# Optimization experiments

Measured on AMD Instinct MI355X. Metric: run time of the kernel, lower is better.

Reference implementation:

```python
import jax, jax.numpy as jnp
import numpy as np

N, D, R, E = 50000, 128, 16, 1600000


def rgcn_conv(x, W, root, bias, src, dst, rel):
    """PyG-style RGCNConv (aggr='mean', root weight + bias).
    out[i] = x[i] @ root + bias + sum_r mean_{j in N_r(i)} x[j] @ W_r
    Aggregate-then-transform: segment-mean per (relation, dst) then contract with W.
    """
    n, d = x.shape
    seg = rel * n + dst  # combined (relation, dst-node) segment id
    msg_sum = jax.ops.segment_sum(x[src], seg, num_segments=R * n).reshape(R, n, d)
    cnt = jax.ops.segment_sum(jnp.ones_like(src, dtype=x.dtype), seg, num_segments=R * n).reshape(R, n, 1)
    msg = msg_sum / jnp.maximum(cnt, 1.0)  # mean aggregation (0 when no edges)
    return jnp.einsum('rnd,rde->ne', msg, W) + x @ root + bias


def setup_inputs() -> dict:
    key = jax.random.key(0)
    ks = jax.random.split(key, 9)
    x = jax.random.normal(ks[0], (N, D), dtype=jnp.float32)
    edge_index = jax.random.randint(ks[1], (2, E), 0, N, dtype=jnp.int64)
    edge_type = jax.random.randint(ks[2], (E,), 0, R, dtype=jnp.int64)
    s = 1.0 / np.sqrt(D)
    W1 = jax.random.normal(ks[3], (R, D, D), dtype=jnp.float32) * s
    root1 = jax.random.normal(ks[4], (D, D), dtype=jnp.float32) * s
    b1 = jnp.zeros((D,), dtype=jnp.float32)
    W2 = jax.random.normal(ks[5], (R, D, D), dtype=jnp.float32) * s
    root2 = jax.random.normal(ks[6], (D, D), dtype=jnp.float32) * s
    b2 = jnp.zeros((D,), dtype=jnp.float32)
    return {"x": x, "edge_index": edge_index, "edge_type": edge_type,
            "W1": W1, "root1": root1, "b1": b1,
            "W2": W2, "root2": root2, "b2": b2}


def reference(x, edge_index, edge_type, W1, root1, b1, W2, root2, b2):
    src, dst = edge_index[0], edge_index[1]
    # layer 1: RGCN -> ReLU -> Dropout (identity in eval mode)
    h = jax.nn.relu(rgcn_conv(x, W1, root1, b1, src, dst, edge_type))
    # layer 2: RGCN -> ReLU
    h = jax.nn.relu(rgcn_conv(h, W2, root2, b2, src, dst, edge_type))
    return h
```

## Files before the change

kernel.cpp:

```cpp
#include <hip/hip_runtime.h>


#define ND 128
#define NR 16
#define KPB 4096

typedef __attribute__((ext_vector_type(8))) short bf16x8;
typedef __attribute__((ext_vector_type(4))) float f32x4;

__device__ __forceinline__ unsigned short f2b(float f) {
    unsigned u = __float_as_uint(f);
    u += 0x7FFFu + ((u >> 16) & 1u);
    return (unsigned short)(u >> 16);
}

__global__ __launch_bounds__(256) void coarse_hist(
    const int* __restrict__ dst, const int* __restrict__ rel,
    int* __restrict__ coarse_cnt, int E, int N, int NBK)
{
    __shared__ int h[1024];
    const int t = threadIdx.x;
    for (int i = t; i < NBK; i += 256) h[i] = 0;
    __syncthreads();
#pragma unroll
    for (int q = 0; q < 16; ++q) {
        int e = blockIdx.x * KPB + q * 256 + t;
        if (e < E) {
            int key = rel[e] * N + dst[e];
            atomicAdd(&h[key >> 12], 1);
        }
    }
    __syncthreads();
    for (int i = t; i < NBK; i += 256)
        if (h[i]) atomicAdd(&coarse_cnt[i], h[i]);
}

__global__ __launch_bounds__(1024) void coarse_scan(
    const int* __restrict__ coarse_cnt, int* __restrict__ cscan,
    int* __restrict__ coarse_cursor, int NBK, int E)
{
    __shared__ int sdata[1024];
    const int t = threadIdx.x;
    int v = (t < NBK) ? coarse_cnt[t] : 0;
    sdata[t] = v;
    __syncthreads();
    for (int off = 1; off < 1024; off <<= 1) {
        int tmp = (t >= off) ? sdata[t - off] : 0;
        __syncthreads();
        sdata[t] += tmp;
        __syncthreads();
    }
    if (t < NBK) {
        int excl = sdata[t] - v;
        cscan[t] = excl;
        coarse_cursor[t] = excl;
    }
    if (t == 0) cscan[NBK] = E;
}

__global__ __launch_bounds__(256) void fillA(
    const int* __restrict__ src, const int* __restrict__ dst,
    const int* __restrict__ rel, int* __restrict__ coarse_cursor,
    uint2* __restrict__ coarse_buf, int E, int N, int NBK)
{
    __shared__ uint2 pairs[KPB];
    __shared__ int h[1024];
    const int t = threadIdx.x;
    for (int i = t; i < NBK; i += 256) h[i] = 0;
    __syncthreads();
#pragma unroll
    for (int q = 0; q < 16; ++q) {
        int e = blockIdx.x * KPB + q * 256 + t;
        unsigned key = 0xFFFFFFFFu, sv = 0;
        if (e < E) {
            key = (unsigned)(rel[e] * N + dst[e]);
            sv = (unsigned)src[e];
            atomicAdd(&h[key >> 12], 1);
        }
        pairs[q * 256 + t] = make_uint2(sv, key);
    }
    __syncthreads();
    for (int i = t; i < NBK; i += 256) {
        int c = h[i];
        h[i] = c ? atomicAdd(&coarse_cursor[i], c) : 0;
    }
    __syncthreads();
#pragma unroll
    for (int q = 0; q < 16; ++q) {
        uint2 p = pairs[q * 256 + t];
        if (p.y != 0xFFFFFFFFu) {
            int pos = atomicAdd(&h[p.y >> 12], 1);
            coarse_buf[pos] = p;
        }
    }
}

__global__ __launch_bounds__(256) void fillB(
    const uint2* __restrict__ coarse_buf, const int* __restrict__ cscan,
    int* __restrict__ seg_off, float* __restrict__ cnt_inv,
    int* __restrict__ sorted_src, int M, int E, int NBK)
{
    __shared__ int cnt[KPB];
    __shared__ int w[256];
    const int t = threadIdx.x;
    const int b = blockIdx.x;
    const int kbase = b << 12;
    const int nkeys = min(KPB, M - kbase);
    const int r0 = cscan[b], r1 = cscan[b + 1];

    for (int i = t; i < KPB; i += 256) cnt[i] = 0;
    __syncthreads();
    for (int e = r0 + t; e < r1; e += 256)
        atomicAdd(&cnt[coarse_buf[e].y - kbase], 1);
    __syncthreads();
    for (int i = t; i < nkeys; i += 256)
        cnt_inv[kbase + i] = 1.0f / fmaxf((float)cnt[i], 1.0f);
    int s = 0;
#pragma unroll
    for (int j = 0; j < 16; ++j) s += cnt[t * 16 + j];
    w[t] = s;
    __syncthreads();
    for (int off = 1; off < 256; off <<= 1) {
        int tmp = (t >= off) ? w[t - off] : 0;
        __syncthreads();
        w[t] += tmp;
        __syncthreads();
    }
    int run = r0 + w[t] - s;
#pragma unroll
    for (int j = 0; j < 16; ++j) {
        int i = t * 16 + j;
        int c = cnt[i];
        cnt[i] = run;
        if (i < nkeys) seg_off[kbase + i] = run;
        run += c;
    }
    if (b == NBK - 1 && t == 0) seg_off[M] = E;
    __syncthreads();
    for (int e = r0 + t; e < r1; e += 256) {
        uint2 p = coarse_buf[e];
        int pos = atomicAdd(&cnt[p.y - kbase], 1);
        sorted_src[pos] = (int)p.x;
    }
}

__global__ __launch_bounds__(256) void conv_x_kernel(
    const float* __restrict__ x, unsigned short* __restrict__ xb, int n4)
{
    int i = blockIdx.x * 256 + threadIdx.x;
    if (i >= n4) return;
    float4 v = ((const float4*)x)[i];
    uint2 o;
    o.x = (unsigned)f2b(v.x) | ((unsigned)f2b(v.y) << 16);
    o.y = (unsigned)f2b(v.z) | ((unsigned)f2b(v.w) << 16);
    ((uint2*)xb)[i] = o;
}

__global__ __launch_bounds__(256) void conv_w_kernel(
    const float* __restrict__ W, const float* __restrict__ root,
    unsigned short* __restrict__ Wt)
{
    int t = blockIdx.x * 256 + threadIdx.x;
    if (t >= 17 * 2048) return;
    int mat = t >> 11;
    int f = t & 2047;
    int lane = f & 63;
    int ctkt = f >> 6;
    int kt = ctkt >> 3;
    int ct = ctkt & 7;
    int n = ct * 16 + (lane & 15);
    int k = kt * 32 + (lane >> 4) * 8;
    const float* s = (mat < 16) ? (W + (size_t)mat * 16384) : root;
    uint4 o;
    o.x = (unsigned)f2b(s[(size_t)(k + 0) * ND + n]) | ((unsigned)f2b(s[(size_t)(k + 1) * ND + n]) << 16);
    o.y = (unsigned)f2b(s[(size_t)(k + 2) * ND + n]) | ((unsigned)f2b(s[(size_t)(k + 3) * ND + n]) << 16);
    o.z = (unsigned)f2b(s[(size_t)(k + 4) * ND + n]) | ((unsigned)f2b(s[(size_t)(k + 5) * ND + n]) << 16);
    o.w = (unsigned)f2b(s[(size_t)(k + 6) * ND + n]) | ((unsigned)f2b(s[(size_t)(k + 7) * ND + n]) << 16);
    *(uint4*)(Wt + (size_t)t * 8) = o;
}

__global__ __launch_bounds__(256) void gather_mean(
    const unsigned short* __restrict__ A,
    const int* __restrict__ seg_off,
    const int* __restrict__ sorted_src,
    const float* __restrict__ cnt_inv,
    unsigned short* __restrict__ msg,
    int N, int r0, int ccN)
{
    int g = blockIdx.x * 16 + (threadIdx.x >> 4);
    if (g >= ccN) return;
    int l = threadIdx.x & 15;
    int s = r0 * N + g;
    int b0 = seg_off[s], e1 = seg_off[s + 1];
    float a0 = 0.f, a1 = 0.f, a2 = 0.f, a3 = 0.f, a4 = 0.f, a5 = 0.f, a6 = 0.f, a7 = 0.f;
    int e = b0;
    for (; e + 2 <= e1; e += 2) {
        int s0 = sorted_src[e];
        int s1 = sorted_src[e + 1];
        uint4 u0 = *(const uint4*)(A + (size_t)s0 * ND + l * 8);
        uint4 u1 = *(const uint4*)(A + (size_t)s1 * ND + l * 8);
        a0 += __uint_as_float(u0.x << 16); a1 += __uint_as_float(u0.x & 0xFFFF0000u);
        a2 += __uint_as_float(u0.y << 16); a3 += __uint_as_float(u0.y & 0xFFFF0000u);
        a4 += __uint_as_float(u0.z << 16); a5 += __uint_as_float(u0.z & 0xFFFF0000u);
        a6 += __uint_as_float(u0.w << 16); a7 += __uint_as_float(u0.w & 0xFFFF0000u);
        a0 += __uint_as_float(u1.x << 16); a1 += __uint_as_float(u1.x & 0xFFFF0000u);
        a2 += __uint_as_float(u1.y << 16); a3 += __uint_as_float(u1.y & 0xFFFF0000u);
        a4 += __uint_as_float(u1.z << 16); a5 += __uint_as_float(u1.z & 0xFFFF0000u);
        a6 += __uint_as_float(u1.w << 16); a7 += __uint_as_float(u1.w & 0xFFFF0000u);
    }
    if (e < e1) {
        int s0 = sorted_src[e];
        uint4 u0 = *(const uint4*)(A + (size_t)s0 * ND + l * 8);
        a0 += __uint_as_float(u0.x << 16); a1 += __uint_as_float(u0.x & 0xFFFF0000u);
        a2 += __uint_as_float(u0.y << 16); a3 += __uint_as_float(u0.y & 0xFFFF0000u);
        a4 += __uint_as_float(u0.z << 16); a5 += __uint_as_float(u0.z & 0xFFFF0000u);
        a6 += __uint_as_float(u0.w << 16); a7 += __uint_as_float(u0.w & 0xFFFF0000u);
    }
    float inv = cnt_inv[s];
    uint4 o;
    o.x = (unsigned)f2b(a0 * inv) | ((unsigned)f2b(a1 * inv) << 16);
    o.y = (unsigned)f2b(a2 * inv) | ((unsigned)f2b(a3 * inv) << 16);
    o.z = (unsigned)f2b(a4 * inv) | ((unsigned)f2b(a5 * inv) << 16);
    o.w = (unsigned)f2b(a6 * inv) | ((unsigned)f2b(a7 * inv) << 16);
    *(uint4*)(msg + (size_t)g * ND + l * 8) = o;
}

__global__ __launch_bounds__(256) void gemm_mfma(
    const unsigned short* __restrict__ msg,
    const unsigned short* __restrict__ xb,
    const unsigned short* __restrict__ Wt,
    const float* __restrict__ bias,
    float* __restrict__ acc_buf,
    unsigned short* __restrict__ out_bf,
    float* __restrict__ out_f32,
    int N, int c0, int cc, int include_root, int load_acc, int finalize)
{
    __shared__ __align__(16) unsigned short Bs[2048 * 8];
    const int tid = threadIdx.x;
    const int lane = tid & 63;
    const int wv = tid >> 6;
    const int quad = lane >> 4;
    const int l16 = lane & 15;
    const int m0 = blockIdx.x * 64 + wv * 16;
    const int arow = m0 + l16;

    f32x4 acc[8];
    if (load_acc) {
#pragma unroll
        for (int ct = 0; ct < 8; ++ct)
#pragma unroll
            for (int rg = 0; rg < 4; ++rg) {
                int r = m0 + quad * 4 + rg;
                acc[ct][rg] = (r < N) ? acc_buf[(size_t)r * ND + ct * 16 + l16] : 0.f;
            }
    } else {
#pragma unroll
        for (int ct = 0; ct < 8; ++ct) { f32x4 z = {0.f, 0.f, 0.f, 0.f}; acc[ct] = z; }
    }

    for (int rel = include_root ? -1 : 0; rel < cc; ++rel) {
        const unsigned short* A = (rel < 0) ? xb : msg + (size_t)rel * N * ND;
        const int mat = (rel < 0) ? 16 : (c0 + rel);
        const uint4* Bsrc = (const uint4*)(Wt + (size_t)mat * 2048 * 8);

        bf16x8 a[4];
#pragma unroll
        for (int kt = 0; kt < 4; ++kt) {
            bf16x8 z = {0, 0, 0, 0, 0, 0, 0, 0};
            a[kt] = (arow < N) ? *(const bf16x8*)(A + (size_t)arow * ND + kt * 32 + quad * 8) : z;
        }

        __syncthreads();
#pragma unroll
        for (int i = 0; i < 8; ++i)
            ((uint4*)Bs)[tid + i * 256] = Bsrc[tid + i * 256];
        __syncthreads();

#pragma unroll
        for (int kt = 0; kt < 4; ++kt) {
#pragma unroll
            for (int ct = 0; ct < 8; ++ct) {
                bf16x8 b = *(const bf16x8*)(Bs + (size_t)((kt * 8 + ct) * 64 + lane) * 8);
                acc[ct] = __builtin_amdgcn_mfma_f32_16x16x32_bf16(a[kt], b, acc[ct], 0, 0, 0);
            }
        }
    }

    if (!finalize) {
#pragma unroll
        for (int ct = 0; ct < 8; ++ct)
#pragma unroll
            for (int rg = 0; rg < 4; ++rg) {
                int r = m0 + quad * 4 + rg;
                if (r < N) acc_buf[(size_t)r * ND + ct * 16 + l16] = acc[ct][rg];
            }
    } else {
#pragma unroll
        for (int ct = 0; ct < 8; ++ct) {
            float bb = bias[ct * 16 + l16];
#pragma unroll
            for (int rg = 0; rg < 4; ++rg) {
                int r = m0 + quad * 4 + rg;
                if (r < N) {
                    float v = fmaxf(acc[ct][rg] + bb, 0.f);
                    if (out_bf) out_bf[(size_t)r * ND + ct * 16 + l16] = f2b(v);
                    else        out_f32[(size_t)r * ND + ct * 16 + l16] = v;
                }
            }
        }
    }
}

extern "C" void kernel_launch(void* const* d_in, const int* in_sizes, int n_in,
                              void* d_out, int out_size, void* d_ws, size_t ws_size,
                              hipStream_t stream) {
    const float* x     = (const float*)d_in[0];
    const int*   eidx  = (const int*)d_in[1];
    const int*   etype = (const int*)d_in[2];
    const float* W1    = (const float*)d_in[3];
    const float* root1 = (const float*)d_in[4];
    const float* b1    = (const float*)d_in[5];
    const float* W2    = (const float*)d_in[6];
    const float* root2 = (const float*)d_in[7];
    const float* b2    = (const float*)d_in[8];
    float* out = (float*)d_out;

    const int N = in_sizes[0] / ND;
    const int E = in_sizes[2];
    const int M = NR * N;
    const int NBK = (M + KPB - 1) / KPB;

    const int* src = eidx;
    const int* dst = eidx + E;

    char* p = (char*)d_ws;
    auto carve = [&](size_t bytes) { char* q = p; p += (bytes + 255) & ~(size_t)255; return q; };
    unsigned short* h_bf    = (unsigned short*)carve((size_t)N * ND * 2);
    unsigned short* x_bf    = (unsigned short*)carve((size_t)N * ND * 2);
    unsigned short* Wt1     = (unsigned short*)carve((size_t)17 * 2048 * 8 * 2);
    unsigned short* Wt2     = (unsigned short*)carve((size_t)17 * 2048 * 8 * 2);
    int*   seg_off          = (int*)  carve((size_t)(M + 1) * 4);
    float* cnt_inv          = (float*)carve((size_t)M * 4);
    int*   sorted_src       = (int*)  carve((size_t)E * 4);
    int*   coarse_cnt       = (int*)  carve(1024 * 4);
    int*   cscan            = (int*)  carve(1025 * 4);
    int*   coarse_cursor    = (int*)  carve(1024 * 4);

    size_t fixed = (size_t)(p - (char*)d_ws);
    size_t remain = (ws_size > fixed) ? ws_size - fixed : 0;
    size_t chunk_bytes = (size_t)N * ND * 2;
    size_t acc_bytes   = (size_t)N * ND * 4;
    int C = 2;
    if (remain >= 16 * chunk_bytes + 512) C = 16;
    else if (remain >= 8 * chunk_bytes + acc_bytes + 512) C = 8;
    else if (remain >= 4 * chunk_bytes + acc_bytes + 512) C = 4;
    uint2* coarse_buf       = (uint2*)p;
    unsigned short* msg     = (unsigned short*)carve((size_t)C * chunk_bytes);
    float* acc              = (float*)((C < 16) ? carve(acc_bytes) : (char*)p);

    const int eb4 = (E + KPB - 1) / KPB;
    const int gemm_blocks = (N + 63) / 64;

    hipMemsetAsync(coarse_cnt, 0, 1024 * 4, stream);
    coarse_hist<<<eb4, 256, 0, stream>>>(dst, etype, coarse_cnt, E, N, NBK);
    coarse_scan<<<1, 1024, 0, stream>>>(coarse_cnt, cscan, coarse_cursor, NBK, E);
    fillA<<<eb4, 256, 0, stream>>>(src, dst, etype, coarse_cursor, coarse_buf, E, N, NBK);
    fillB<<<NBK, 256, 0, stream>>>(coarse_buf, cscan, seg_off, cnt_inv, sorted_src, M, E, NBK);

    conv_x_kernel<<<((N * ND / 4) + 255) / 256, 256, 0, stream>>>(x, x_bf, N * ND / 4);
    conv_w_kernel<<<(17 * 2048 + 255) / 256, 256, 0, stream>>>(W1, root1, Wt1);
    conv_w_kernel<<<(17 * 2048 + 255) / 256, 256, 0, stream>>>(W2, root2, Wt2);

    for (int layer = 0; layer < 2; ++layer) {
        const unsigned short* A  = (layer == 0) ? x_bf : h_bf;
        const unsigned short* Wt = (layer == 0) ? Wt1  : Wt2;
        const float* biasp       = (layer == 0) ? b1   : b2;

        for (int c0 = 0; c0 < NR; c0 += C) {
            int cc = (NR - c0 < C) ? (NR - c0) : C;
            int ccN = cc * N;
            gather_mean<<<(ccN + 15) / 16, 256, 0, stream>>>(
                A, seg_off, sorted_src, cnt_inv, msg, N, c0, ccN);
            int fin = (c0 + cc == NR) ? 1 : 0;
            gemm_mfma<<<gemm_blocks, 256, 0, stream>>>(
                msg, A, Wt, biasp, acc,
                (fin && layer == 0) ? h_bf : (unsigned short*)nullptr,
                (fin && layer == 1) ? out : (float*)nullptr,
                N, c0, cc, c0 == 0 ? 1 : 0, c0 > 0 ? 1 : 0, fin);
        }
    }
}
```

Before: 521.1 us.

## Split GEMM output columns across wave pairs and load weights directly into LDS

Each block of the MFMA GEMM now covers 32 rows instead of 64. Pairs of waves share a 16-row tile, each wave computing half of the output columns, which halves the accumulator registers per wave and doubles the block count. The launch bound now requests more resident blocks per CU. Weight tiles are copied with global_load_lds straight into shared memory instead of passing through registers, and final fp32 outputs use nontemporal stores. The trade-off is that each block now loads the full 32KB weight tile to produce half as many rows, doubling total weight traffic through LDS. The A fragments are also loaded redundantly by both waves of a pair.

```diff
diff --git a/kernel.cpp b/kernel.cpp
--- a/kernel.cpp
+++ b/kernel.cpp
@@ -12,6 +12,12 @@
     unsigned u = __float_as_uint(f);
     u += 0x7FFFu + ((u >> 16) & 1u);
     return (unsigned short)(u >> 16);
+}
+
+__device__ __forceinline__ void gload16(const unsigned short* g, unsigned short* l) {
+    __builtin_amdgcn_global_load_lds(
+        (__attribute__((address_space(1))) void*)g,
+        (__attribute__((address_space(3))) void*)l, 16, 0, 0);
 }
 
 __global__ __launch_bounds__(256) void coarse_hist(
@@ -225,7 +231,7 @@
     *(uint4*)(msg + (size_t)g * ND + l * 8) = o;
 }
 
-__global__ __launch_bounds__(256) void gemm_mfma(
+__global__ __launch_bounds__(256, 5) void gemm_mfma(
     const unsigned short* __restrict__ msg,
     const unsigned short* __restrict__ xb,
     const unsigned short* __restrict__ Wt,
@@ -239,72 +245,83 @@
     const int tid = threadIdx.x;
     const int lane = tid & 63;
     const int wv = tid >> 6;
+    const int rg = wv >> 1;
+    const int ch = wv & 1;
     const int quad = lane >> 4;
     const int l16 = lane & 15;
-    const int m0 = blockIdx.x * 64 + wv * 16;
+    const int m0 = blockIdx.x * 32 + rg * 16;
     const int arow = m0 + l16;
 
-    f32x4 acc[8];
+    f32x4 acc[4];
     if (load_acc) {
 #pragma unroll
-        for (int ct = 0; ct < 8; ++ct)
-#pragma unroll
-            for (int rg = 0; rg < 4; ++rg) {
-                int r = m0 + quad * 4 + rg;
-                acc[ct][rg] = (r < N) ? acc_buf[(size_t)r * ND + ct * 16 + l16] : 0.f;
+        for (int c = 0; c < 4; ++c) {
+            int ct = ch * 4 + c;
+#pragma unroll
+            for (int rgi = 0; rgi < 4; ++rgi) {
+                int r = m0 + quad * 4 + rgi;
+                acc[c][rgi] = (r < N) ? acc_buf[(size_t)r * ND + ct * 16 + l16] : 0.f;
             }
+        }
     } else {
 #pragma unroll
-        for (int ct = 0; ct < 8; ++ct) { f32x4 z = {0.f, 0.f, 0.f, 0.f}; acc[ct] = z; }
-    }
-
-    for (int rel = include_root ? -1 : 0; rel < cc; ++rel) {
-        const unsigned short* A = (rel < 0) ? xb : msg + (size_t)rel * N * ND;
+        for (int c = 0; c < 4; ++c) { f32x4 z = {0.f, 0.f, 0.f, 0.f}; acc[c] = z; }
+    }
+
+    const int rel0 = include_root ? -1 : 0;
+    const bf16x8 zfrag = {0, 0, 0, 0, 0, 0, 0, 0};
+
+    for (int rel = rel0; rel < cc; ++rel) {
+        const unsigned short* A = (rel < 0) ? xb : msg + (size_t)rel * (size_t)N * ND;
         const int mat = (rel < 0) ? 16 : (c0 + rel);
-        const uint4* Bsrc = (const uint4*)(Wt + (size_t)mat * 2048 * 8);
+        const unsigned short* Bsrc = Wt + (size_t)mat * 2048 * 8;
 
         bf16x8 a[4];
 #pragma unroll
         for (int kt = 0; kt < 4; ++kt) {
-            bf16x8 z = {0, 0, 0, 0, 0, 0, 0, 0};
-            a[kt] = (arow < N) ? *(const bf16x8*)(A + (size_t)arow * ND + kt * 32 + quad * 8) : z;
+            const bf16x8* ap = (const bf16x8*)(A + (size_t)arow * ND + kt * 32 + quad * 8);
+            a[kt] = (arow < N) ? *ap : zfrag;
         }
 
         __syncthreads();
 #pragma unroll
         for (int i = 0; i < 8; ++i)
-            ((uint4*)Bs)[tid + i * 256] = Bsrc[tid + i * 256];
+            gload16(Bsrc + (size_t)(tid + i * 256) * 8, &Bs[(size_t)(tid + i * 256) * 8]);
         __syncthreads();
 
 #pragma unroll
         for (int kt = 0; kt < 4; ++kt) {
 #pragma unroll
-            for (int ct = 0; ct < 8; ++ct) {
+            for (int c = 0; c < 4; ++c) {
+                int ct = ch * 4 + c;
                 bf16x8 b = *(const bf16x8*)(Bs + (size_t)((kt * 8 + ct) * 64 + lane) * 8);
-                acc[ct] = __builtin_amdgcn_mfma_f32_16x16x32_bf16(a[kt], b, acc[ct], 0, 0, 0);
+                acc[c] = __builtin_amdgcn_mfma_f32_16x16x32_bf16(a[kt], b, acc[c], 0, 0, 0);
             }
         }
     }
 
     if (!finalize) {
 #pragma unroll
-        for (int ct = 0; ct < 8; ++ct)
-#pragma unroll
-            for (int rg = 0; rg < 4; ++rg) {
-                int r = m0 + quad * 4 + rg;
-                if (r < N) acc_buf[(size_t)r * ND + ct * 16 + l16] = acc[ct][rg];
+        for (int c = 0; c < 4; ++c) {
+            int ct = ch * 4 + c;
+#pragma unroll
+            for (int rgi = 0; rgi < 4; ++rgi) {
+                int r = m0 + quad * 4 + rgi;
+                if (r < N) acc_buf[(size_t)r * ND + ct * 16 + l16] = acc[c][rgi];
             }
+        }
     } else {
 #pragma unroll
-        for (int ct = 0; ct < 8; ++ct) {
+        for (int c = 0; c < 4; ++c) {
+            int ct = ch * 4 + c;
             float bb = bias[ct * 16 + l16];
 #pragma unroll
-            for (int rg = 0; rg < 4; ++rg) {
-                int r = m0 + quad * 4 + rg;
+            for (int rgi = 0; rgi < 4; ++rgi) {
+                int r = m0 + quad * 4 + rgi;
                 if (r < N) {
-                    float v = fmaxf(acc[ct][rg] + bb, 0.f);
+                    float v = fmaxf(acc[c][rgi] + bb, 0.f);
                     if (out_bf) out_bf[(size_t)r * ND + ct * 16 + l16] = f2b(v);
-                    else        out_f32[(size_t)r * ND + ct * 16 + l16] = v;
+                    else        __builtin_nontemporal_store(v, &out_f32[(size_t)r * ND + ct * 16 + l16]);
                 }
             }
         }
@@ -359,7 +376,7 @@
     float* acc              = (float*)((C < 16) ? carve(acc_bytes) : (char*)p);
 
     const int eb4 = (E + KPB - 1) / KPB;
-    const int gemm_blocks = (N + 63) / 64;
+    const int gemm_blocks = (N + 31) / 32;
 
     hipMemsetAsync(coarse_cnt, 0, 1024 * 4, stream);
     coarse_hist<<<eb4, 256, 0, stream>>>(dst, etype, coarse_cnt, E, N, NBK);
```

Measured after the change: 547.5 us. 5.1% more time.

## Double-buffer weight tiles in LDS with async global-to-LDS loads in GEMM

Applied to the files above, without the earlier changes.

Rewrites the per-relation loop of the MFMA GEMM as a two-stage software pipeline. Two LDS buffers are used, and the next relation's weight tile is loaded with global_load_lds (plus the next A fragments into registers) while the current one is being multiplied. This hides global-load latency behind MFMA work. It doubles the LDS footprint per block, which can lower occupancy, and it relies on the barrier waiting for the async LDS loads. The final fp32 output store is also switched to nontemporal.

```diff
diff --git a/kernel.cpp b/kernel.cpp
--- a/kernel.cpp
+++ b/kernel.cpp
@@ -12,6 +12,12 @@
     unsigned u = __float_as_uint(f);
     u += 0x7FFFu + ((u >> 16) & 1u);
     return (unsigned short)(u >> 16);
+}
+
+__device__ __forceinline__ void gload16(const unsigned short* g, unsigned short* l) {
+    __builtin_amdgcn_global_load_lds(
+        (__attribute__((address_space(1))) void*)g,
+        (__attribute__((address_space(3))) void*)l, 16, 0, 0);
 }
 
 __global__ __launch_bounds__(256) void coarse_hist(
@@ -225,6 +231,32 @@
     *(uint4*)(msg + (size_t)g * ND + l * 8) = o;
 }
 
+#define PREFETCH(ph, BS, areg) do {                                              \
+    const int rel_ = rel0 + (ph);                                                \
+    const unsigned short* A_ = (rel_ < 0) ? xb : msg + (size_t)rel_ * (size_t)N * ND; \
+    const int mat_ = (rel_ < 0) ? 16 : (c0 + rel_);                              \
+    const unsigned short* Bsrc_ = Wt + (size_t)mat_ * 2048 * 8;                  \
+    _Pragma("unroll")                                                            \
+    for (int i_ = 0; i_ < 8; ++i_)                                               \
+        gload16(Bsrc_ + (size_t)(tid + i_ * 256) * 8, BS + (size_t)(tid + i_ * 256) * 8); \
+    _Pragma("unroll")                                                            \
+    for (int kt_ = 0; kt_ < 4; ++kt_) {                                          \
+        const bf16x8* ap_ = (const bf16x8*)(A_ + (size_t)arow * ND + kt_ * 32 + quad * 8); \
+        areg[kt_] = (arow < N) ? *ap_ : zfrag;                                   \
+    }                                                                            \
+} while (0)
+
+#define COMPUTE(BS, areg) do {                                                   \
+    _Pragma("unroll")                                                            \
+    for (int kt_ = 0; kt_ < 4; ++kt_) {                                          \
+        _Pragma("unroll")                                                        \
+        for (int ct_ = 0; ct_ < 8; ++ct_) {                                      \
+            bf16x8 b_ = *(const bf16x8*)(BS + (size_t)((kt_ * 8 + ct_) * 64 + lane) * 8); \
+            acc[ct_] = __builtin_amdgcn_mfma_f32_16x16x32_bf16(areg[kt_], b_, acc[ct_], 0, 0, 0); \
+        }                                                                        \
+    }                                                                            \
+} while (0)
+
 __global__ __launch_bounds__(256) void gemm_mfma(
     const unsigned short* __restrict__ msg,
     const unsigned short* __restrict__ xb,
@@ -235,7 +267,8 @@
     float* __restrict__ out_f32,
     int N, int c0, int cc, int include_root, int load_acc, int finalize)
 {
-    __shared__ __align__(16) unsigned short Bs[2048 * 8];
+    __shared__ __align__(16) unsigned short Bs0[2048 * 8];
+    __shared__ __align__(16) unsigned short Bs1[2048 * 8];
     const int tid = threadIdx.x;
     const int lane = tid & 63;
     const int wv = tid >> 6;
@@ -258,32 +291,26 @@
         for (int ct = 0; ct < 8; ++ct) { f32x4 z = {0.f, 0.f, 0.f, 0.f}; acc[ct] = z; }
     }
 
-    for (int rel = include_root ? -1 : 0; rel < cc; ++rel) {
-        const unsigned short* A = (rel < 0) ? xb : msg + (size_t)rel * N * ND;
-        const int mat = (rel < 0) ? 16 : (c0 + rel);
-        const uint4* Bsrc = (const uint4*)(Wt + (size_t)mat * 2048 * 8);
-
-        bf16x8 a[4];
-#pragma unroll
-        for (int kt = 0; kt < 4; ++kt) {
-            bf16x8 z = {0, 0, 0, 0, 0, 0, 0, 0};
-            a[kt] = (arow < N) ? *(const bf16x8*)(A + (size_t)arow * ND + kt * 32 + quad * 8) : z;
-        }
-
-        __syncthreads();
-#pragma unroll
-        for (int i = 0; i < 8; ++i)
-            ((uint4*)Bs)[tid + i * 256] = Bsrc[tid + i * 256];
-        __syncthreads();
-
-#pragma unroll
-        for (int kt = 0; kt < 4; ++kt) {
-#pragma unroll
-            for (int ct = 0; ct < 8; ++ct) {
-                bf16x8 b = *(const bf16x8*)(Bs + (size_t)((kt * 8 + ct) * 64 + lane) * 8);
-                acc[ct] = __builtin_amdgcn_mfma_f32_16x16x32_bf16(a[kt], b, acc[ct], 0, 0, 0);
-            }
-        }
+    const int rel0 = include_root ? -1 : 0;
+    const int P = cc - rel0;
+    const bf16x8 zfrag = {0, 0, 0, 0, 0, 0, 0, 0};
+    bf16x8 a0[4], a1[4];
+
+    PREFETCH(0, Bs0, a0);
+    int p = 0;
+    for (; p + 2 <= P; p += 2) {
+        __syncthreads();
+        if (p + 1 < P) { PREFETCH(p + 1, Bs1, a1); }
+        __builtin_amdgcn_sched_barrier(0);
+        COMPUTE(Bs0, a0);
+        __syncthreads();
+        if (p + 2 < P) { PREFETCH(p + 2, Bs0, a0); }
+        __builtin_amdgcn_sched_barrier(0);
+        COMPUTE(Bs1, a1);
+    }
+    if (p < P) {
+        __syncthreads();
+        COMPUTE(Bs0, a0);
     }
 
     if (!finalize) {
@@ -304,7 +331,7 @@
                 if (r < N) {
                     float v = fmaxf(acc[ct][rg] + bb, 0.f);
                     if (out_bf) out_bf[(size_t)r * ND + ct * 16 + l16] = f2b(v);
-                    else        out_f32[(size_t)r * ND + ct * 16 + l16] = v;
+                    else        __builtin_nontemporal_store(v, &out_f32[(size_t)r * ND + ct * 16 + l16]);
                 }
             }
         }
```

Result: faster. 500.4 us (-4.0%).
